# Performance work log

Hardware: AMD Instinct MI355X
Metric: run time of the kernel (lower is better)

Reference implementation:

```python
import jax, jax.numpy as jnp
import numpy as np
import math

B, S, H, DM, DH = 4, 1024, 12, 768, 64


def setup_inputs() -> dict:
    key = jax.random.key(0)
    ks = jax.random.split(key, 5)
    std = 0.02
    return {
        "normalized_resid_pre": jax.random.normal(ks[0], (B, S, H, DM), dtype=jnp.float32),
        "W_Q": jax.random.normal(ks[1], (H, DM, DH), dtype=jnp.float32) * std,
        "b_Q": jnp.zeros((H, DH), dtype=jnp.float32),
        "W_K": jax.random.normal(ks[2], (H, DM, DH), dtype=jnp.float32) * std,
        "b_K": jnp.zeros((H, DH), dtype=jnp.float32),
        "W_V": jax.random.normal(ks[3], (H, DM, DH), dtype=jnp.float32) * std,
        "b_V": jnp.zeros((H, DH), dtype=jnp.float32),
        "W_O": jax.random.normal(ks[4], (H, DH, DM), dtype=jnp.float32) * std,
        "b_O": jnp.zeros((DM,), dtype=jnp.float32),
    }


def reference(normalized_resid_pre, W_Q, b_Q, W_K, b_K, W_V, b_V, W_O, b_O):
    x = normalized_resid_pre  # [B, S, H, DM]
    q = jnp.einsum("bshm,hmd->bshd", x, W_Q) + b_Q  # [B,S,H,DH]
    k = jnp.einsum("bshm,hmd->bshd", x, W_K) + b_K
    v = jnp.einsum("bshm,hmd->bshd", x, W_V) + b_V
    # positional_embedding_type == 'learned' -> no rotary applied
    scores = jnp.einsum("bqhd,bkhd->bhqk", q, k) / math.sqrt(DH)  # [B,H,S,S]
    causal = jnp.triu(jnp.ones((S, S), dtype=bool), k=1)  # True above diagonal
    scores = jnp.where(causal[None, None], -jnp.inf, scores)
    pattern = jax.nn.softmax(scores, axis=-1)
    pattern = jnp.where(jnp.isnan(pattern), 0.0, pattern)
    z = jnp.einsum("bhqk,bkhd->bqhd", pattern, v)  # [B,S,H,DH]
    # NOTE: per-head output (no sum over heads), bias split across heads
    attn_out = jnp.einsum("bqhd,hdm->bqhm", z, W_O) + b_O / H  # [B,S,H,DM]
    return attn_out
```

## Files before the change

### kernel.cpp

```cpp
#include <hip/hip_runtime.h>
#include <hip/hip_bf16.h>
#include <stdint.h>

constexpr int CB = 4, CS = 1024, CH = 12, CDM = 768, CDH = 64;
constexpr float QSCALE = 0.125f * 1.44269504088896340736f;
constexpr float SHIFT = 4.0f;

typedef __attribute__((ext_vector_type(8))) short bf16x8;
typedef __attribute__((ext_vector_type(4))) float f32x4;

__device__ inline short f2bf(float f) {
    union { __hip_bfloat16 h; short s; } u;
    u.h = __float2bfloat16(f);
    return u.s;
}
__device__ inline float exp2fast(float f) { return __builtin_amdgcn_exp2f(f); }

__global__ __launch_bounds__(256) void prep_kernel(
    const float* __restrict__ wq, const float* __restrict__ wk,
    const float* __restrict__ wv, const float* __restrict__ wo,
    short* __restrict__ wT, short* __restrict__ woT)
{
    const int blk = blockIdx.x;
    __shared__ short tile[64 * 65];
    const int tid = threadIdx.x;

    if (blk < 3 * CH * (CDM / 64)) {
        const int wsel = blk / (CH * (CDM / 64));
        const int rem = blk % (CH * (CDM / 64));
        const int h = rem / (CDM / 64);
        const int m0 = (rem % (CDM / 64)) * 64;
        const float* wp = (wsel == 0) ? wq : (wsel == 1) ? wk : wv;
        const float scale = (wsel == 0) ? QSCALE : 1.0f;
        #pragma unroll
        for (int it = 0; it < 16; ++it) {
            int i = it * 4 + (tid >> 6);
            int d = tid & 63;
            tile[i * 65 + d] = f2bf(wp[((size_t)h * CDM + m0 + i) * CDH + d] * scale);
        }
        __syncthreads();
        #pragma unroll
        for (int it = 0; it < 16; ++it) {
            int d = it * 4 + (tid >> 6);
            int m = tid & 63;
            wT[((size_t)(wsel * CH + h) * CDH + d) * CDM + m0 + m] = tile[m * 65 + d];
        }
    } else {
        const int r2 = blk - 3 * CH * (CDM / 64);
        const int h = r2 / (CDM / 64);
        const int m0 = (r2 % (CDM / 64)) * 64;
        #pragma unroll
        for (int it = 0; it < 16; ++it) {
            int d = it * 4 + (tid >> 6);
            int m = tid & 63;
            tile[m * 65 + d] = f2bf(wo[((size_t)h * CDH + d) * CDM + m0 + m]);
        }
        __syncthreads();
        #pragma unroll
        for (int it = 0; it < 16; ++it) {
            int m = it * 4 + (tid >> 6);
            int d = tid & 63;
            woT[((size_t)h * CDM + m0 + m) * CDH + d] = tile[m * 65 + d];
        }
    }
}

__global__ __launch_bounds__(256) void qkv_kernel(
    const float* __restrict__ x, const short* __restrict__ wT,
    const float* __restrict__ bq, const float* __restrict__ bk,
    const float* __restrict__ bv,
    short* __restrict__ q_ws, short* __restrict__ k_ws, short* __restrict__ vt_ws)
{
    const int h = blockIdx.y;
    const int row0 = blockIdx.x * 64;
    const int tid = threadIdx.x;
    const int w = tid >> 6;
    const int l = tid & 63;
    const int l15 = l & 15, lg = l >> 4;

    __shared__ short sbuf[2 * 12288];

    const f32x4 zero4 = {0.f, 0.f, 0.f, 0.f};
    f32x4 acc[12];
    #pragma unroll
    for (int i = 0; i < 12; ++i) acc[i] = zero4;

    const float* xrow = x + (size_t)(row0 + w * 16 + l15) * (CH * CDM) + h * CDM + lg * 8;

    const int r_lo = tid >> 3;
    const int s_phys = tid & 7;
    auto stage = [&](int bsel, int kk) {
        #pragma unroll
        for (int j = 0; j < 6; ++j) {
            int r = j * 32 + r_lo;
            int s_log = s_phys ^ (r & 7);
            const short* gp = wT + ((size_t)((r >> 6) * CH + h) * CDH + (r & 63)) * CDM
                              + kk + s_log * 8;
            short* lp = sbuf + bsel * 12288 + (j * 4096 + w * 1024) / 2;
            __builtin_amdgcn_global_load_lds(
                (const __attribute__((address_space(1))) uint32_t*)gp,
                (__attribute__((address_space(3))) uint32_t*)lp, 16, 0, 0);
        }
    };

    float4 xp0 = *(const float4*)(xrow);
    float4 xp1 = *(const float4*)(xrow + 4);
    float4 xp2 = *(const float4*)(xrow + 32);
    float4 xp3 = *(const float4*)(xrow + 36);
    stage(0, 0);
    asm volatile("s_waitcnt vmcnt(0)" ::: "memory");
    __syncthreads();

    for (int t = 0; t < 12; ++t) {
        const int kk = t * 64;
        bf16x8 A0, A1;
        A0[0] = f2bf(xp0.x); A0[1] = f2bf(xp0.y); A0[2] = f2bf(xp0.z); A0[3] = f2bf(xp0.w);
        A0[4] = f2bf(xp1.x); A0[5] = f2bf(xp1.y); A0[6] = f2bf(xp1.z); A0[7] = f2bf(xp1.w);
        A1[0] = f2bf(xp2.x); A1[1] = f2bf(xp2.y); A1[2] = f2bf(xp2.z); A1[3] = f2bf(xp2.w);
        A1[4] = f2bf(xp3.x); A1[5] = f2bf(xp3.y); A1[6] = f2bf(xp3.z); A1[7] = f2bf(xp3.w);

        if (t < 11) stage((t + 1) & 1, kk + 64);
        __builtin_amdgcn_sched_barrier(0);
        if (t < 11) {
            xp0 = *(const float4*)(xrow + kk + 64);
            xp1 = *(const float4*)(xrow + kk + 68);
            xp2 = *(const float4*)(xrow + kk + 96);
            xp3 = *(const float4*)(xrow + kk + 100);
        }

        const short* bb = sbuf + (t & 1) * 12288;
        #pragma unroll
        for (int ct = 0; ct < 12; ++ct) {
            int r = ct * 16 + l15;
            int sw = r & 7;
            bf16x8 b0 = *(const bf16x8*)(bb + r * 64 + ((lg ^ sw) << 3));
            bf16x8 b1 = *(const bf16x8*)(bb + r * 64 + (((4 | lg) ^ sw) << 3));
            acc[ct] = __builtin_amdgcn_mfma_f32_16x16x32_bf16(A0, b0, acc[ct], 0, 0, 0);
            acc[ct] = __builtin_amdgcn_mfma_f32_16x16x32_bf16(A1, b1, acc[ct], 0, 0, 0);
        }
        asm volatile("s_waitcnt vmcnt(4)" ::: "memory");
        __syncthreads();
    }

    const int b = row0 >> 10;
    const int sbase = row0 & (CS - 1);
    const size_t qkbase = (size_t)(b * CH + h) * CS;
    short* vt = sbuf;

    #pragma unroll
    for (int t = 0; t < 4; ++t) {
        int d = t * 16 + l15;
        float biasq = bq[h * CDH + d] * QSCALE;
        float biask = bk[h * CDH + d];
        float biasv = bv[h * CDH + d];
        #pragma unroll
        for (int r = 0; r < 4; ++r) {
            int s = sbase + w * 16 + lg * 4 + r;
            q_ws[(qkbase + s) * CDH + d] = f2bf(acc[t][r] + biasq);
            k_ws[(qkbase + s) * CDH + d] = f2bf(acc[4 + t][r] + biask);
            vt[d * 72 + (w * 16 + lg * 4 + r)] = f2bf(acc[8 + t][r] + biasv);
        }
    }
    __syncthreads();
    {
        int dd = tid >> 2;
        int s0 = (tid & 3) * 16;
        size_t vdst = ((size_t)(b * CH + h) * CDH + dd) * CS + sbase + s0;
        *(bf16x8*)(vt_ws + vdst)     = *(const bf16x8*)(&vt[dd * 72 + s0]);
        *(bf16x8*)(vt_ws + vdst + 8) = *(const bf16x8*)(&vt[dd * 72 + s0 + 8]);
    }
}

__global__ __launch_bounds__(256) void attn_out_kernel(
    const short* __restrict__ q_ws, const short* __restrict__ k_ws,
    const short* __restrict__ vt_ws, const short* __restrict__ woT,
    const float* __restrict__ bo, float* __restrict__ out)
{
    const int f = blockIdx.x;
    const int xcd = f & 7;
    const int s = f >> 3;
    const int r_rank = (s < 32) ? s : (s < 64 ? 95 - s : s);
    const int c = 15 - (r_rank / 6);
    const int bh = xcd + 8 * (r_rank % 6);
    const int b = bh / CH, h = bh % CH;
    const int tid = threadIdx.x;
    const int wv = tid >> 6, l = tid & 63;
    const int l15 = l & 15, lg = l >> 4;
    const int q0w = c * 64 + wv * 16;

    __shared__ short kvbuf[2][8192];
    __shared__ short pls_all[4][16 * 72];

    short* pls = &pls_all[wv][0];
    const short* kg = k_ws + (size_t)bh * CS * CDH;
    const short* vg = vt_ws + (size_t)bh * CDH * CS;

    const short* qp = q_ws + ((size_t)bh * CS + q0w + l15) * CDH + lg * 8;
    bf16x8 aq0 = *(const bf16x8*)(qp);
    bf16x8 aq1 = *(const bf16x8*)(qp + 32);

    const f32x4 zero4 = {0.f, 0.f, 0.f, 0.f};
    f32x4 acc_o[4];
    #pragma unroll
    for (int j = 0; j < 4; ++j) acc_o[j] = zero4;
    float l_r[4] = {0.f, 0.f, 0.f, 0.f};

    auto stage = [&](int bsel, int t) {
        #pragma unroll
        for (int j = 0; j < 2; ++j) {
            int slot = j * 256 + tid;
            int row = slot >> 3;
            int sl = (slot & 7) ^ (row & 7);
            const short* gk = kg + (size_t)(t * 64 + row) * CDH + sl * 8;
            const short* gv = vg + (size_t)row * CS + t * 64 + sl * 8;
            short* lk = &kvbuf[bsel][(j * 256 + wv * 64) * 8];
            short* lv = &kvbuf[bsel][4096 + (j * 256 + wv * 64) * 8];
            __builtin_amdgcn_global_load_lds(
                (const __attribute__((address_space(1))) uint32_t*)gk,
                (__attribute__((address_space(3))) uint32_t*)lk, 16, 0, 0);
            __builtin_amdgcn_global_load_lds(
                (const __attribute__((address_space(1))) uint32_t*)gv,
                (__attribute__((address_space(3))) uint32_t*)lv, 16, 0, 0);
        }
    };

    const int T = c + 1;

    stage(0, 0);
    asm volatile("s_waitcnt vmcnt(0)" ::: "memory");
    __syncthreads();

    for (int t = 0; t < T; ++t) {
        if (t + 1 < T) stage((t + 1) & 1, t + 1);

        const short* kb = kvbuf[t & 1];
        const short* vb = kvbuf[t & 1] + 4096;
        bf16x8 kf[4][2], vf[4][2];
        #pragma unroll
        for (int j = 0; j < 4; ++j) {
            int row = j * 16 + l15, sw = row & 7;
            kf[j][0] = *(const bf16x8*)(kb + row * 64 + ((lg ^ sw) << 3));
            kf[j][1] = *(const bf16x8*)(kb + row * 64 + (((4 | lg) ^ sw) << 3));
        }
        #pragma unroll
        for (int ct = 0; ct < 4; ++ct) {
            int row = ct * 16 + l15, sw = row & 7;
            vf[ct][0] = *(const bf16x8*)(vb + row * 64 + ((lg ^ sw) << 3));
            vf[ct][1] = *(const bf16x8*)(vb + row * 64 + (((4 | lg) ^ sw) << 3));
        }

        f32x4 s4[4];
        __builtin_amdgcn_s_setprio(1);
        #pragma unroll
        for (int j = 0; j < 4; ++j) {
            s4[j] = __builtin_amdgcn_mfma_f32_16x16x32_bf16(aq0, kf[j][0], zero4, 0, 0, 0);
            s4[j] = __builtin_amdgcn_mfma_f32_16x16x32_bf16(aq1, kf[j][1], s4[j], 0, 0, 0);
        }
        __builtin_amdgcn_s_setprio(0);
        if (t == T - 1) {
            #pragma unroll
            for (int j = 0; j < 4; ++j)
                #pragma unroll
                for (int r = 0; r < 4; ++r)
                    if (t * 64 + j * 16 + l15 > q0w + lg * 4 + r)
                        s4[j][r] = -1e30f;
        }
        #pragma unroll
        for (int r = 0; r < 4; ++r) {
            float p0 = exp2fast(s4[0][r] - SHIFT);
            float p1 = exp2fast(s4[1][r] - SHIFT);
            float p2 = exp2fast(s4[2][r] - SHIFT);
            float p3 = exp2fast(s4[3][r] - SHIFT);
            l_r[r] += (p0 + p1) + (p2 + p3);
            short* pr = pls + (lg * 4 + r) * 72 + l15;
            pr[0]  = f2bf(p0);
            pr[16] = f2bf(p1);
            pr[32] = f2bf(p2);
            pr[48] = f2bf(p3);
        }
        asm volatile("s_waitcnt lgkmcnt(0)" ::: "memory");
        bf16x8 pa0 = *(const bf16x8*)(&pls[l15 * 72 + lg * 8]);
        bf16x8 pa1 = *(const bf16x8*)(&pls[l15 * 72 + 32 + lg * 8]);
        __builtin_amdgcn_s_setprio(1);
        #pragma unroll
        for (int ct = 0; ct < 4; ++ct) {
            acc_o[ct] = __builtin_amdgcn_mfma_f32_16x16x32_bf16(pa0, vf[ct][0], acc_o[ct], 0, 0, 0);
            acc_o[ct] = __builtin_amdgcn_mfma_f32_16x16x32_bf16(pa1, vf[ct][1], acc_o[ct], 0, 0, 0);
        }
        __builtin_amdgcn_s_setprio(0);

        asm volatile("s_waitcnt vmcnt(0)" ::: "memory");
        __syncthreads();
    }

    #pragma unroll
    for (int r = 0; r < 4; ++r) {
        float rs = l_r[r];
        rs += __shfl_xor(rs, 1);
        rs += __shfl_xor(rs, 2);
        rs += __shfl_xor(rs, 4);
        rs += __shfl_xor(rs, 8);
        float inv = 1.0f / rs;
        short* zr = pls + (lg * 4 + r) * 72 + l15;
        zr[0]  = f2bf(acc_o[0][r] * inv);
        zr[16] = f2bf(acc_o[1][r] * inv);
        zr[32] = f2bf(acc_o[2][r] * inv);
        zr[48] = f2bf(acc_o[3][r] * inv);
    }
    asm volatile("s_waitcnt lgkmcnt(0)" ::: "memory");
    bf16x8 a0 = *(const bf16x8*)(&pls[l15 * 72 + lg * 8]);
    bf16x8 a1 = *(const bf16x8*)(&pls[l15 * 72 + 32 + lg * 8]);

    const short* wo_h = woT + (size_t)h * CDM * CDH;
    float* obase = out + ((size_t)(b * CS + q0w) * CH + h) * CDM;
    float* fst = (float*)(&kvbuf[0][0]) + (size_t)wv * (16 * 68);

    for (int ch = 0; ch < 12; ++ch) {
        asm volatile("s_waitcnt lgkmcnt(0)" ::: "memory");
        #pragma unroll
        for (int ct2 = 0; ct2 < 4; ++ct2) {
            int ct = ch * 4 + ct2;
            const short* wb = wo_h + (size_t)(ct * 16 + l15) * CDH + lg * 8;
            bf16x8 b0 = *(const bf16x8*)(wb);
            bf16x8 b1 = *(const bf16x8*)(wb + 32);
            f32x4 acc = __builtin_amdgcn_mfma_f32_16x16x32_bf16(a0, b0, zero4, 0, 0, 0);
            acc = __builtin_amdgcn_mfma_f32_16x16x32_bf16(a1, b1, acc, 0, 0, 0);
            float bias = bo[ct * 16 + l15] * (1.0f / CH);
            #pragma unroll
            for (int r = 0; r < 4; ++r)
                fst[(lg * 4 + r) * 68 + ct2 * 16 + l15] = acc[r] + bias;
        }
        asm volatile("s_waitcnt lgkmcnt(0)" ::: "memory");
        #pragma unroll
        for (int it = 0; it < 4; ++it) {
            int idx = it * 64 + l;
            int row = idx >> 4;
            int c4 = idx & 15;
            float4 v = *(const float4*)(fst + row * 68 + c4 * 4);
            *(float4*)(obase + (size_t)row * (CH * CDM) + ch * 64 + c4 * 4) = v;
        }
    }
}

extern "C" void kernel_launch(void* const* d_in, const int* in_sizes, int n_in,
                              void* d_out, int out_size, void* d_ws, size_t ws_size,
                              hipStream_t stream) {
    const float* x  = (const float*)d_in[0];
    const float* wq = (const float*)d_in[1];
    const float* bq = (const float*)d_in[2];
    const float* wk = (const float*)d_in[3];
    const float* bk = (const float*)d_in[4];
    const float* wv = (const float*)d_in[5];
    const float* bv = (const float*)d_in[6];
    const float* wo = (const float*)d_in[7];
    const float* bo = (const float*)d_in[8];
    float* out = (float*)d_out;

    const size_t tsz = (size_t)CB * CH * CS * CDH;
    short* q_ws  = (short*)d_ws;
    short* k_ws  = q_ws + tsz;
    short* vt_ws = k_ws + tsz;
    short* z_ws  = vt_ws + tsz;
    short* wT  = z_ws;
    short* woT = z_ws + (size_t)3 * CH * CDH * CDM;

    prep_kernel<<<dim3(4 * CH * (CDM / 64)), 256, 0, stream>>>(
        wq, wk, wv, wo, wT, woT);
    qkv_kernel<<<dim3(CB * CS / 64, CH), 256, 0, stream>>>(
        x, wT, bq, bk, bv, q_ws, k_ws, vt_ws);
    attn_out_kernel<<<dim3(16 * CB * CH), 256, 0, stream>>>(
        q_ws, k_ws, vt_ws, woT, bo, out);
}
```

Before: 115.7 us.

## Compute transposed scores so P feeds PV MFMA from registers, skip LDS round-trip

Swaps the MFMA operands so the score tile comes out transposed (key index in registers, query in lanes). Each lane's probabilities then form the A operand of 16x16x16 bf16 MFMAs directly, with no write to LDS and reload. V fragments are reloaded as 4-element pieces to match, and the causal mask and row-sum reduction are rewritten for the new layout. This trades the per-tile LDS store, wait and load for twice as many smaller MFMAs and more, narrower V LDS reads.

```diff
diff --git a/kernel.cpp b/kernel.cpp
--- a/kernel.cpp
+++ b/kernel.cpp
@@ -7,6 +7,7 @@
 constexpr float SHIFT = 4.0f;
 
 typedef __attribute__((ext_vector_type(8))) short bf16x8;
+typedef __attribute__((ext_vector_type(4))) short bf16x4;
 typedef __attribute__((ext_vector_type(4))) float f32x4;
 
 __device__ inline short f2bf(float f) {
@@ -203,7 +204,7 @@
     f32x4 acc_o[4];
     #pragma unroll
     for (int j = 0; j < 4; ++j) acc_o[j] = zero4;
-    float l_r[4] = {0.f, 0.f, 0.f, 0.f};
+    float l_r = 0.f;
 
     auto stage = [&](int bsel, int t) {
         #pragma unroll
@@ -235,26 +236,29 @@
 
         const short* kb = kvbuf[t & 1];
         const short* vb = kvbuf[t & 1] + 4096;
-        bf16x8 kf[4][2], vf[4][2];
+        bf16x8 kf[4][2];
         #pragma unroll
         for (int j = 0; j < 4; ++j) {
             int row = j * 16 + l15, sw = row & 7;
             kf[j][0] = *(const bf16x8*)(kb + row * 64 + ((lg ^ sw) << 3));
             kf[j][1] = *(const bf16x8*)(kb + row * 64 + (((4 | lg) ^ sw) << 3));
         }
-        #pragma unroll
-        for (int ct = 0; ct < 4; ++ct) {
-            int row = ct * 16 + l15, sw = row & 7;
-            vf[ct][0] = *(const bf16x8*)(vb + row * 64 + ((lg ^ sw) << 3));
-            vf[ct][1] = *(const bf16x8*)(vb + row * 64 + (((4 | lg) ^ sw) << 3));
-        }
+        bf16x4 vf16[4][4];
+        #pragma unroll
+        for (int j = 0; j < 4; ++j)
+            #pragma unroll
+            for (int ct = 0; ct < 4; ++ct) {
+                int row = ct * 16 + l15;
+                int slot = (2 * j + (lg >> 1)) ^ (row & 7);
+                vf16[j][ct] = *(const bf16x4*)(vb + row * 64 + slot * 8 + 4 * (lg & 1));
+            }
 
         f32x4 s4[4];
         __builtin_amdgcn_s_setprio(1);
         #pragma unroll
         for (int j = 0; j < 4; ++j) {
-            s4[j] = __builtin_amdgcn_mfma_f32_16x16x32_bf16(aq0, kf[j][0], zero4, 0, 0, 0);
-            s4[j] = __builtin_amdgcn_mfma_f32_16x16x32_bf16(aq1, kf[j][1], s4[j], 0, 0, 0);
+            s4[j] = __builtin_amdgcn_mfma_f32_16x16x32_bf16(kf[j][0], aq0, zero4, 0, 0, 0);
+            s4[j] = __builtin_amdgcn_mfma_f32_16x16x32_bf16(kf[j][1], aq1, s4[j], 0, 0, 0);
         }
         __builtin_amdgcn_s_setprio(0);
         if (t == T - 1) {
@@ -262,50 +266,47 @@
             for (int j = 0; j < 4; ++j)
                 #pragma unroll
                 for (int r = 0; r < 4; ++r)
-                    if (t * 64 + j * 16 + l15 > q0w + lg * 4 + r)
+                    if (t * 64 + j * 16 + lg * 4 + r > q0w + l15)
                         s4[j][r] = -1e30f;
         }
-        #pragma unroll
-        for (int r = 0; r < 4; ++r) {
-            float p0 = exp2fast(s4[0][r] - SHIFT);
-            float p1 = exp2fast(s4[1][r] - SHIFT);
-            float p2 = exp2fast(s4[2][r] - SHIFT);
-            float p3 = exp2fast(s4[3][r] - SHIFT);
-            l_r[r] += (p0 + p1) + (p2 + p3);
-            short* pr = pls + (lg * 4 + r) * 72 + l15;
-            pr[0]  = f2bf(p0);
-            pr[16] = f2bf(p1);
-            pr[32] = f2bf(p2);
-            pr[48] = f2bf(p3);
-        }
-        asm volatile("s_waitcnt lgkmcnt(0)" ::: "memory");
-        bf16x8 pa0 = *(const bf16x8*)(&pls[l15 * 72 + lg * 8]);
-        bf16x8 pa1 = *(const bf16x8*)(&pls[l15 * 72 + 32 + lg * 8]);
+        bf16x4 pj[4];
+        #pragma unroll
+        for (int j = 0; j < 4; ++j) {
+            float p0 = exp2fast(s4[j][0] - SHIFT);
+            float p1 = exp2fast(s4[j][1] - SHIFT);
+            float p2 = exp2fast(s4[j][2] - SHIFT);
+            float p3 = exp2fast(s4[j][3] - SHIFT);
+            l_r += (p0 + p1) + (p2 + p3);
+            pj[j][0] = f2bf(p0); pj[j][1] = f2bf(p1);
+            pj[j][2] = f2bf(p2); pj[j][3] = f2bf(p3);
+        }
         __builtin_amdgcn_s_setprio(1);
         #pragma unroll
-        for (int ct = 0; ct < 4; ++ct) {
-            acc_o[ct] = __builtin_amdgcn_mfma_f32_16x16x32_bf16(pa0, vf[ct][0], acc_o[ct], 0, 0, 0);
-            acc_o[ct] = __builtin_amdgcn_mfma_f32_16x16x32_bf16(pa1, vf[ct][1], acc_o[ct], 0, 0, 0);
-        }
+        for (int j = 0; j < 4; ++j)
+            #pragma unroll
+            for (int ct = 0; ct < 4; ++ct)
+                acc_o[ct] = __builtin_amdgcn_mfma_f32_16x16x16bf16_1k(
+                    pj[j], vf16[j][ct], acc_o[ct], 0, 0, 0);
         __builtin_amdgcn_s_setprio(0);
 
         asm volatile("s_waitcnt vmcnt(0)" ::: "memory");
         __syncthreads();
     }
 
+    float rs = l_r;
+    rs += __shfl_xor(rs, 16);
+    rs += __shfl_xor(rs, 32);
+    float invq[4];
+    #pragma unroll
+    for (int r = 0; r < 4; ++r) invq[r] = 1.0f / __shfl(rs, lg * 4 + r);
+
     #pragma unroll
     for (int r = 0; r < 4; ++r) {
-        float rs = l_r[r];
-        rs += __shfl_xor(rs, 1);
-        rs += __shfl_xor(rs, 2);
-        rs += __shfl_xor(rs, 4);
-        rs += __shfl_xor(rs, 8);
-        float inv = 1.0f / rs;
         short* zr = pls + (lg * 4 + r) * 72 + l15;
-        zr[0]  = f2bf(acc_o[0][r] * inv);
-        zr[16] = f2bf(acc_o[1][r] * inv);
-        zr[32] = f2bf(acc_o[2][r] * inv);
-        zr[48] = f2bf(acc_o[3][r] * inv);
+        zr[0]  = f2bf(acc_o[0][r] * invq[r]);
+        zr[16] = f2bf(acc_o[1][r] * invq[r]);
+        zr[32] = f2bf(acc_o[2][r] * invq[r]);
+        zr[48] = f2bf(acc_o[3][r] * invq[r]);
     }
     asm volatile("s_waitcnt lgkmcnt(0)" ::: "memory");
     bf16x8 a0 = *(const bf16x8*)(&pls[l15 * 72 + lg * 8]);
```

Result: no change. 114.7 us (-0.9%).
